# Performance work log

Measured on AMD Instinct MI355X. Metric: run time of the kernel, lower is better.

## Reference

```python
import jax, jax.numpy as jnp
import numpy as np


def setup_inputs() -> dict:
    key = jax.random.key(0)
    k1, k2, k3 = jax.random.split(key, 3)
    IN_C, OUT_C, K = 64, 64, 3
    x = jax.random.normal(k1, (16, IN_C, 256, 256), dtype=jnp.float32)
    # Conv2d weight (OIHW) and bias, Kaiming-ish scale
    fan_in = IN_C * K * K
    W = jax.random.normal(k2, (OUT_C, IN_C, K, K), dtype=jnp.float32) / np.sqrt(fan_in).astype(np.float32)
    b = jax.random.normal(k3, (OUT_C,), dtype=jnp.float32) * 0.01
    return {"x": x, "W": W, "b": b}


def reference(x, W, b):
    # The original module's quadruple Python loop multiplies each pixel by
    # mask(=1) * (1 - (h-1==h and w-1==w)) == 1, i.e. it is an identity.
    # The faithful math is therefore exactly Conv2d(k=3, padding=1) + bias.
    out = jax.lax.conv_general_dilated(
        x, W,
        window_strides=(1, 1),
        padding=((1, 1), (1, 1)),
        dimension_numbers=("NCHW", "OIHW", "NCHW"),
    )
    return out + b[None, :, None, None]
```

## Files before the change

kernel.cpp:

```cpp
#include <hip/hip_runtime.h>


#define N_   16
#define C_   64
#define HW_  256
#define TH   8
#define TW   32
#define NPIX ((TH + 2) * (TW + 2))
#define ICP  72

typedef __attribute__((ext_vector_type(8)))  short short8;
typedef __attribute__((ext_vector_type(16))) float f32x16;

static __device__ __forceinline__ unsigned short f2bf(float f) {
    unsigned u = __builtin_bit_cast(unsigned, f);
    return (unsigned short)((u + 0x7fffu + ((u >> 16) & 1u)) >> 16);
}

__global__ void repack_w_bf16(const float* __restrict__ W, unsigned short* __restrict__ Wt) {
    int i = blockIdx.x * 256 + threadIdx.x;
    if (i < C_ * 9 * C_) {
        int ic = i & 63, tap = (i >> 6) % 9, oc = (i >> 6) / 9;
        Wt[i] = f2bf(W[(oc * C_ + ic) * 9 + tap]);
    }
}

__global__ __launch_bounds__(256) void transpose_nhwc(const float* __restrict__ x,
                                                      unsigned short* __restrict__ xt) {
    __shared__ unsigned short st[64][ICP];
    const int tid = threadIdx.x;
    const int w0  = blockIdx.x * 64;
    const int h   = blockIdx.y;
    const int n   = blockIdx.z;

    #pragma unroll
    for (int k = 0; k < 4; ++k) {
        int i  = tid + k * 256;
        int ic = i >> 4, seg = i & 15;
        float4 v = *(const float4*)(x + (((size_t)(n * C_ + ic) * HW_ + h) * HW_ + w0 + seg * 4));
        st[seg * 4 + 0][ic] = f2bf(v.x);
        st[seg * 4 + 1][ic] = f2bf(v.y);
        st[seg * 4 + 2][ic] = f2bf(v.z);
        st[seg * 4 + 3][ic] = f2bf(v.w);
    }
    __syncthreads();
    #pragma unroll
    for (int j = 0; j < 2; ++j) {
        int w = (tid >> 3) + 32 * j, eg = tid & 7;
        uint4 v = *(const uint4*)&st[w][eg * 8];
        *(uint4*)(xt + (((size_t)n * HW_ + h) * HW_ + w0 + w) * C_ + eg * 8) = v;
    }
}

__global__ __launch_bounds__(256, 3) void conv_mfma_nhwc(const unsigned short* __restrict__ xt,
                                                         const unsigned short* __restrict__ Wt,
                                                         const float* __restrict__ bias,
                                                         float* __restrict__ out) {
    __shared__ unsigned short sx[NPIX][ICP];

    const int tid  = threadIdx.x;
    const int L    = tid & 63, wv = tid >> 6;
    const int half = L >> 5,  lm = L & 31;
    const int w0 = blockIdx.x * TW, h0 = blockIdx.y * TH, n = blockIdx.z;

    const unsigned short* xtn = xt + (size_t)n * HW_ * HW_ * C_;
    #pragma unroll
    for (int k = 0; k < 11; ++k) {
        int i = tid + k * 256;
        if (i < NPIX * 8) {
            int p = i >> 3, e = i & 7;
            int r = p / 34, col = p - r * 34;
            int gh = h0 + r - 1, gw = w0 + col - 1;
            uint4 v = make_uint4(0, 0, 0, 0);
            if ((unsigned)gh < HW_ && (unsigned)gw < HW_)
                v = *(const uint4*)(xtn + ((size_t)gh * HW_ + gw) * C_ + e * 8);
            *(uint4*)&sx[p][e * 8] = v;
        }
    }

    f32x16 acc00, acc01, acc10, acc11;
    #pragma unroll
    for (int r = 0; r < 16; ++r) {
        int ro = (r & 3) + 8 * (r >> 2) + 4 * half;
        float b0 = bias[ro], b1 = bias[32 + ro];
        acc00[r] = b0; acc01[r] = b0;
        acc10[r] = b1; acc11[r] = b1;
    }
    __syncthreads();

    const int r0 = 2 * wv;
    const unsigned short* wr0 = Wt + (0 * 32 + lm) * 576;
    const unsigned short* wr1 = Wt + (1 * 32 + lm) * 576;

    #pragma unroll
    for (int kh = 0; kh < 3; ++kh) {
        #pragma unroll
        for (int kw = 0; kw < 3; ++kw) {
            const int tap = kh * 3 + kw;
            const unsigned short* a0p = wr0 + tap * 64;
            const unsigned short* a1p = wr1 + tap * 64;
            const unsigned short* b0p = &sx[(r0 + kh) * 34 + lm + kw][0];
            const unsigned short* b1p = &sx[(r0 + 1 + kh) * 34 + lm + kw][0];
            #pragma unroll
            for (int s = 0; s < 4; ++s) {
                const int eo = s * 16 + half * 8;
                short8 a0 = __builtin_bit_cast(short8, *(const uint4*)(a0p + eo));
                short8 a1 = __builtin_bit_cast(short8, *(const uint4*)(a1p + eo));
                short8 b0 = __builtin_bit_cast(short8, *(const uint4*)(b0p + eo));
                short8 b1 = __builtin_bit_cast(short8, *(const uint4*)(b1p + eo));
                acc00 = __builtin_amdgcn_mfma_f32_32x32x16_bf16(a0, b0, acc00, 0, 0, 0);
                acc01 = __builtin_amdgcn_mfma_f32_32x32x16_bf16(a0, b1, acc01, 0, 0, 0);
                acc10 = __builtin_amdgcn_mfma_f32_32x32x16_bf16(a1, b0, acc10, 0, 0, 0);
                acc11 = __builtin_amdgcn_mfma_f32_32x32x16_bf16(a1, b1, acc11, 0, 0, 0);
            }
        }
    }

    float* outn = out + (size_t)n * C_ * HW_ * HW_;
    #pragma unroll
    for (int r = 0; r < 16; ++r) {
        int ro = (r & 3) + 8 * (r >> 2) + 4 * half;
        size_t base0 = ((size_t)ro        * HW_ + (h0 + r0)) * HW_ + w0 + lm;
        size_t base1 = ((size_t)(32 + ro) * HW_ + (h0 + r0)) * HW_ + w0 + lm;
        outn[base0]       = acc00[r];
        outn[base0 + HW_] = acc01[r];
        outn[base1]       = acc10[r];
        outn[base1 + HW_] = acc11[r];
    }
}

__global__ __launch_bounds__(256, 3) void conv_mfma_f32src(const float* __restrict__ x,
                                                           const unsigned short* __restrict__ Wt,
                                                           const float* __restrict__ bias,
                                                           float* __restrict__ out) {
    __shared__ unsigned short sx[NPIX][ICP];
    const int tid  = threadIdx.x;
    const int L    = tid & 63, wv = tid >> 6;
    const int half = L >> 5,  lm = L & 31;
    const int w0 = blockIdx.x * TW, h0 = blockIdx.y * TH, n = blockIdx.z;

    f32x16 acc00, acc01, acc10, acc11;
    #pragma unroll
    for (int r = 0; r < 16; ++r) {
        int ro = (r & 3) + 8 * (r >> 2) + 4 * half;
        float b0 = bias[ro], b1 = bias[32 + ro];
        acc00[r] = b0; acc01[r] = b0;
        acc10[r] = b1; acc11[r] = b1;
    }

    const float* xn = x + (size_t)n * C_ * HW_ * HW_;
    for (int c = tid; c < NPIX * 32; c += 256) {
        int icp = c / NPIX;
        int p   = c - icp * NPIX;
        int ph  = p / 34;
        int gh  = h0 + ph - 1, gw = w0 + (p - ph * 34) - 1;
        float v0 = 0.f, v1 = 0.f;
        if ((unsigned)gh < HW_ && (unsigned)gw < HW_) {
            const float* px = xn + ((size_t)(icp * 2) * HW_ + gh) * HW_ + gw;
            v0 = px[0];
            v1 = px[HW_ * HW_];
        }
        unsigned pk = (unsigned)f2bf(v0) | ((unsigned)f2bf(v1) << 16);
        *(unsigned*)&sx[p][icp * 2] = pk;
    }
    __syncthreads();

    const int r0 = 2 * wv;
    const unsigned short* wr0 = Wt + (0 * 32 + lm) * 576;
    const unsigned short* wr1 = Wt + (1 * 32 + lm) * 576;
    #pragma unroll
    for (int kh = 0; kh < 3; ++kh) {
        #pragma unroll
        for (int kw = 0; kw < 3; ++kw) {
            const int tap = kh * 3 + kw;
            const unsigned short* a0p = wr0 + tap * 64;
            const unsigned short* a1p = wr1 + tap * 64;
            const unsigned short* b0p = &sx[(r0 + kh) * 34 + lm + kw][0];
            const unsigned short* b1p = &sx[(r0 + 1 + kh) * 34 + lm + kw][0];
            #pragma unroll
            for (int s = 0; s < 4; ++s) {
                const int eo = s * 16 + half * 8;
                short8 a0 = __builtin_bit_cast(short8, *(const uint4*)(a0p + eo));
                short8 a1 = __builtin_bit_cast(short8, *(const uint4*)(a1p + eo));
                short8 b0 = __builtin_bit_cast(short8, *(const uint4*)(b0p + eo));
                short8 b1 = __builtin_bit_cast(short8, *(const uint4*)(b1p + eo));
                acc00 = __builtin_amdgcn_mfma_f32_32x32x16_bf16(a0, b0, acc00, 0, 0, 0);
                acc01 = __builtin_amdgcn_mfma_f32_32x32x16_bf16(a0, b1, acc01, 0, 0, 0);
                acc10 = __builtin_amdgcn_mfma_f32_32x32x16_bf16(a1, b0, acc10, 0, 0, 0);
                acc11 = __builtin_amdgcn_mfma_f32_32x32x16_bf16(a1, b1, acc11, 0, 0, 0);
            }
        }
    }

    float* outn = out + (size_t)n * C_ * HW_ * HW_;
    #pragma unroll
    for (int r = 0; r < 16; ++r) {
        int ro = (r & 3) + 8 * (r >> 2) + 4 * half;
        size_t base0 = ((size_t)ro        * HW_ + (h0 + r0)) * HW_ + w0 + lm;
        size_t base1 = ((size_t)(32 + ro) * HW_ + (h0 + r0)) * HW_ + w0 + lm;
        outn[base0]       = acc00[r];
        outn[base0 + HW_] = acc01[r];
        outn[base1]       = acc10[r];
        outn[base1 + HW_] = acc11[r];
    }
}

extern "C" void kernel_launch(void* const* d_in, const int* in_sizes, int n_in,
                              void* d_out, int out_size, void* d_ws, size_t ws_size,
                              hipStream_t stream) {
    const float* x = (const float*)d_in[0];
    const float* W = (const float*)d_in[1];
    const float* b = (const float*)d_in[2];
    float* out = (float*)d_out;

    dim3 grid(HW_ / TW, HW_ / TH, N_);
    dim3 block(256);

    const size_t xt_bytes = (size_t)N_ * HW_ * HW_ * C_ * sizeof(unsigned short);
    const size_t wt_bytes = (size_t)C_ * 9 * C_ * sizeof(unsigned short);

    if (ws_size >= xt_bytes + wt_bytes) {
        unsigned short* xt = (unsigned short*)d_ws;
        unsigned short* Wt = (unsigned short*)d_ws + xt_bytes / 2;
        repack_w_bf16<<<(C_ * 9 * C_ + 255) / 256, 256, 0, stream>>>(W, Wt);
        transpose_nhwc<<<dim3(4, HW_, N_), 256, 0, stream>>>(x, xt);
        conv_mfma_nhwc<<<grid, block, 0, stream>>>(xt, Wt, b, out);
    } else if (ws_size >= wt_bytes) {
        unsigned short* Wt = (unsigned short*)d_ws;
        repack_w_bf16<<<(C_ * 9 * C_ + 255) / 256, 256, 0, stream>>>(W, Wt);
        conv_mfma_f32src<<<grid, block, 0, stream>>>(x, Wt, b, out);
    }
}
```

Before: 644.3 us.

## Make conv persistent over row tiles with register-resident weights and prefetch

The conv kernel now runs 512-thread blocks that each loop over eight consecutive 8-row tiles. Each wave keeps its 32-output-channel weight slice in registers, and the next halo tile is prefetched into registers while the current one is computed, then written to shared memory between barriers. This cuts repeated weight loads from global memory and per-block launch and halo overhead. The transpose kernel also now packs channel pairs and uses an XOR-swizzled shared layout to reduce bank conflicts. In exchange the kernel carries a large register footprint (36 short8 weight fragments plus staging buffers), which may limit occupancy or cause spills.

Measured after the change: 588.8 us. 8.6% less time.

```diff
diff --git a/kernel.cpp b/kernel.cpp
--- a/kernel.cpp
+++ b/kernel.cpp
@@ -8,6 +8,7 @@
 #define TW   32
 #define NPIX ((TH + 2) * (TW + 2))
 #define ICP  72
+#define NT   8
 
 typedef __attribute__((ext_vector_type(8)))  short short8;
 typedef __attribute__((ext_vector_type(16))) float f32x16;
@@ -33,26 +34,35 @@
     const int h   = blockIdx.y;
     const int n   = blockIdx.z;
 
-    #pragma unroll
-    for (int k = 0; k < 4; ++k) {
-        int i  = tid + k * 256;
-        int ic = i >> 4, seg = i & 15;
-        float4 v = *(const float4*)(x + (((size_t)(n * C_ + ic) * HW_ + h) * HW_ + w0 + seg * 4));
-        st[seg * 4 + 0][ic] = f2bf(v.x);
-        st[seg * 4 + 1][ic] = f2bf(v.y);
-        st[seg * 4 + 2][ic] = f2bf(v.z);
-        st[seg * 4 + 3][ic] = f2bf(v.w);
+    const int seg = tid & 7;
+    const int icp = tid >> 3;
+    const int c   = icp >> 2, q = icp & 3;
+
+    #pragma unroll
+    for (int k = 0; k < 2; ++k) {
+        const float* p0 = x + (((size_t)(n * C_ + 2 * icp) * HW_ + h) * HW_ + w0 + k * 32 + seg * 4);
+        float4 a = *(const float4*)p0;
+        float4 b = *(const float4*)(p0 + (size_t)HW_ * HW_);
+        unsigned pk0 = (unsigned)f2bf(a.x) | ((unsigned)f2bf(b.x) << 16);
+        unsigned pk1 = (unsigned)f2bf(a.y) | ((unsigned)f2bf(b.y) << 16);
+        unsigned pk2 = (unsigned)f2bf(a.z) | ((unsigned)f2bf(b.z) << 16);
+        unsigned pk3 = (unsigned)f2bf(a.w) | ((unsigned)f2bf(b.w) << 16);
+        const int wb = k * 32 + seg * 4;
+        *(unsigned*)&st[wb + 0][(c ^ ((wb + 0) & 7)) * 8 + q * 2] = pk0;
+        *(unsigned*)&st[wb + 1][(c ^ ((wb + 1) & 7)) * 8 + q * 2] = pk1;
+        *(unsigned*)&st[wb + 2][(c ^ ((wb + 2) & 7)) * 8 + q * 2] = pk2;
+        *(unsigned*)&st[wb + 3][(c ^ ((wb + 3) & 7)) * 8 + q * 2] = pk3;
     }
     __syncthreads();
     #pragma unroll
     for (int j = 0; j < 2; ++j) {
         int w = (tid >> 3) + 32 * j, eg = tid & 7;
-        uint4 v = *(const uint4*)&st[w][eg * 8];
+        uint4 v = *(const uint4*)&st[w][(eg ^ (w & 7)) * 8];
         *(uint4*)(xt + (((size_t)n * HW_ + h) * HW_ + w0 + w) * C_ + eg * 8) = v;
     }
 }
 
-__global__ __launch_bounds__(256, 3) void conv_mfma_nhwc(const unsigned short* __restrict__ xt,
+__global__ __launch_bounds__(512, 2) void conv_mfma_wreg(const unsigned short* __restrict__ xt,
                                                          const unsigned short* __restrict__ Wt,
                                                          const float* __restrict__ bias,
                                                          float* __restrict__ out) {
@@ -61,71 +71,118 @@
     const int tid  = threadIdx.x;
     const int L    = tid & 63, wv = tid >> 6;
     const int half = L >> 5,  lm = L & 31;
-    const int w0 = blockIdx.x * TW, h0 = blockIdx.y * TH, n = blockIdx.z;
-
-    const unsigned short* xtn = xt + (size_t)n * HW_ * HW_ * C_;
-    #pragma unroll
-    for (int k = 0; k < 11; ++k) {
-        int i = tid + k * 256;
-        if (i < NPIX * 8) {
-            int p = i >> 3, e = i & 7;
-            int r = p / 34, col = p - r * 34;
-            int gh = h0 + r - 1, gw = w0 + col - 1;
-            uint4 v = make_uint4(0, 0, 0, 0);
-            if ((unsigned)gh < HW_ && (unsigned)gw < HW_)
-                v = *(const uint4*)(xtn + ((size_t)gh * HW_ + gw) * C_ + e * 8);
-            *(uint4*)&sx[p][e * 8] = v;
-        }
-    }
-
-    f32x16 acc00, acc01, acc10, acc11;
+    const int mg   = wv >> 2;
+    const int ng   = wv & 3;
+
+    const int bx = blockIdx.x;
+    const int wt = bx & 7, hg = (bx >> 3) & 3, n = bx >> 5;
+    const int w0 = wt * TW;
+
+    short8 wf[9][4];
+    {
+        const unsigned short* wbase = Wt + (size_t)(32 * mg + lm) * 576 + half * 8;
+        #pragma unroll
+        for (int tap = 0; tap < 9; ++tap)
+            #pragma unroll
+            for (int s = 0; s < 4; ++s)
+                wf[tap][s] = __builtin_bit_cast(short8, *(const uint4*)(wbase + tap * 64 + s * 16));
+    }
+    f32x16 bias_v;
     #pragma unroll
     for (int r = 0; r < 16; ++r) {
         int ro = (r & 3) + 8 * (r >> 2) + 4 * half;
-        float b0 = bias[ro], b1 = bias[32 + ro];
-        acc00[r] = b0; acc01[r] = b0;
-        acc10[r] = b1; acc11[r] = b1;
-    }
-    __syncthreads();
-
-    const int r0 = 2 * wv;
-    const unsigned short* wr0 = Wt + (0 * 32 + lm) * 576;
-    const unsigned short* wr1 = Wt + (1 * 32 + lm) * 576;
-
-    #pragma unroll
-    for (int kh = 0; kh < 3; ++kh) {
+        bias_v[r] = bias[32 * mg + ro];
+    }
+
+    const unsigned short* xtn = xt + (size_t)n * HW_ * HW_ * C_;
+    float* outn = out + (size_t)n * C_ * HW_ * HW_;
+    const unsigned short* pB = &sx[2 * ng * 34 + lm][half * 8];
+
+    {
+        const int h0 = hg * (NT * TH);
+        #pragma unroll
+        for (int k = 0; k < 6; ++k) {
+            int i = tid + k * 512;
+            if (i < NPIX * 8) {
+                int p = i >> 3, e = i & 7;
+                int r = p / 34, col = p - r * 34;
+                int gh = h0 + r - 1, gw = w0 + col - 1;
+                uint4 v = make_uint4(0, 0, 0, 0);
+                if ((unsigned)gh < HW_ && (unsigned)gw < HW_)
+                    v = *(const uint4*)(xtn + ((size_t)gh * HW_ + gw) * C_ + e * 8);
+                *(uint4*)&sx[p][e * 8] = v;
+            }
+        }
+    }
+    asm volatile("s_waitcnt lgkmcnt(0)" ::: "memory");
+    __builtin_amdgcn_sched_barrier(0);
+    __builtin_amdgcn_s_barrier();
+    __builtin_amdgcn_sched_barrier(0);
+
+    for (int t = 0; t < NT; ++t) {
+        const int h0 = hg * (NT * TH) + t * TH;
+
+        uint4 stg[6];
+        if (t < NT - 1) {
+            const int h1 = h0 + TH;
+            #pragma unroll
+            for (int k = 0; k < 6; ++k) {
+                int i = tid + k * 512;
+                stg[k] = make_uint4(0, 0, 0, 0);
+                if (i < NPIX * 8) {
+                    int p = i >> 3, e = i & 7;
+                    int r = p / 34, col = p - r * 34;
+                    int gh = h1 + r - 1, gw = w0 + col - 1;
+                    if ((unsigned)gh < HW_ && (unsigned)gw < HW_)
+                        stg[k] = *(const uint4*)(xtn + ((size_t)gh * HW_ + gw) * C_ + e * 8);
+                }
+            }
+        }
+
+        f32x16 acc0 = bias_v, acc1 = bias_v;
         #pragma unroll
         for (int kw = 0; kw < 3; ++kw) {
-            const int tap = kh * 3 + kw;
-            const unsigned short* a0p = wr0 + tap * 64;
-            const unsigned short* a1p = wr1 + tap * 64;
-            const unsigned short* b0p = &sx[(r0 + kh) * 34 + lm + kw][0];
-            const unsigned short* b1p = &sx[(r0 + 1 + kh) * 34 + lm + kw][0];
             #pragma unroll
             for (int s = 0; s < 4; ++s) {
-                const int eo = s * 16 + half * 8;
-                short8 a0 = __builtin_bit_cast(short8, *(const uint4*)(a0p + eo));
-                short8 a1 = __builtin_bit_cast(short8, *(const uint4*)(a1p + eo));
-                short8 b0 = __builtin_bit_cast(short8, *(const uint4*)(b0p + eo));
-                short8 b1 = __builtin_bit_cast(short8, *(const uint4*)(b1p + eo));
-                acc00 = __builtin_amdgcn_mfma_f32_32x32x16_bf16(a0, b0, acc00, 0, 0, 0);
-                acc01 = __builtin_amdgcn_mfma_f32_32x32x16_bf16(a0, b1, acc01, 0, 0, 0);
-                acc10 = __builtin_amdgcn_mfma_f32_32x32x16_bf16(a1, b0, acc10, 0, 0, 0);
-                acc11 = __builtin_amdgcn_mfma_f32_32x32x16_bf16(a1, b1, acc11, 0, 0, 0);
-            }
-        }
-    }
-
-    float* outn = out + (size_t)n * C_ * HW_ * HW_;
-    #pragma unroll
-    for (int r = 0; r < 16; ++r) {
-        int ro = (r & 3) + 8 * (r >> 2) + 4 * half;
-        size_t base0 = ((size_t)ro        * HW_ + (h0 + r0)) * HW_ + w0 + lm;
-        size_t base1 = ((size_t)(32 + ro) * HW_ + (h0 + r0)) * HW_ + w0 + lm;
-        outn[base0]       = acc00[r];
-        outn[base0 + HW_] = acc01[r];
-        outn[base1]       = acc10[r];
-        outn[base1 + HW_] = acc11[r];
+                short8 q0 = __builtin_bit_cast(short8, *(const uint4*)(pB + (0 * 34 + kw) * ICP + s * 16));
+                short8 q1 = __builtin_bit_cast(short8, *(const uint4*)(pB + (1 * 34 + kw) * ICP + s * 16));
+                short8 q2 = __builtin_bit_cast(short8, *(const uint4*)(pB + (2 * 34 + kw) * ICP + s * 16));
+                short8 q3 = __builtin_bit_cast(short8, *(const uint4*)(pB + (3 * 34 + kw) * ICP + s * 16));
+                acc0 = __builtin_amdgcn_mfma_f32_32x32x16_bf16(wf[0 * 3 + kw][s], q0, acc0, 0, 0, 0);
+                acc1 = __builtin_amdgcn_mfma_f32_32x32x16_bf16(wf[0 * 3 + kw][s], q1, acc1, 0, 0, 0);
+                acc0 = __builtin_amdgcn_mfma_f32_32x32x16_bf16(wf[1 * 3 + kw][s], q1, acc0, 0, 0, 0);
+                acc1 = __builtin_amdgcn_mfma_f32_32x32x16_bf16(wf[1 * 3 + kw][s], q2, acc1, 0, 0, 0);
+                acc0 = __builtin_amdgcn_mfma_f32_32x32x16_bf16(wf[2 * 3 + kw][s], q2, acc0, 0, 0, 0);
+                acc1 = __builtin_amdgcn_mfma_f32_32x32x16_bf16(wf[2 * 3 + kw][s], q3, acc1, 0, 0, 0);
+            }
+        }
+
+        const int row0 = h0 + 2 * ng;
+        #pragma unroll
+        for (int r = 0; r < 16; ++r) {
+            int ro = (r & 3) + 8 * (r >> 2) + 4 * half;
+            size_t base = ((size_t)(32 * mg + ro) * HW_ + row0) * HW_ + w0 + lm;
+            outn[base]       = acc0[r];
+            outn[base + HW_] = acc1[r];
+        }
+
+        if (t < NT - 1) {
+            __builtin_amdgcn_sched_barrier(0);
+            __builtin_amdgcn_s_barrier();
+            __builtin_amdgcn_sched_barrier(0);
+            #pragma unroll
+            for (int k = 0; k < 6; ++k) {
+                int i = tid + k * 512;
+                if (i < NPIX * 8) {
+                    int p = i >> 3, e = i & 7;
+                    *(uint4*)&sx[p][e * 8] = stg[k];
+                }
+            }
+            asm volatile("s_waitcnt lgkmcnt(0)" ::: "memory");
+            __builtin_amdgcn_sched_barrier(0);
+            __builtin_amdgcn_s_barrier();
+            __builtin_amdgcn_sched_barrier(0);
+        }
     }
 }
 
@@ -213,9 +270,6 @@
     const float* b = (const float*)d_in[2];
     float* out = (float*)d_out;
 
-    dim3 grid(HW_ / TW, HW_ / TH, N_);
-    dim3 block(256);
-
     const size_t xt_bytes = (size_t)N_ * HW_ * HW_ * C_ * sizeof(unsigned short);
     const size_t wt_bytes = (size_t)C_ * 9 * C_ * sizeof(unsigned short);
 
@@ -224,10 +278,10 @@
         unsigned short* Wt = (unsigned short*)d_ws + xt_bytes / 2;
         repack_w_bf16<<<(C_ * 9 * C_ + 255) / 256, 256, 0, stream>>>(W, Wt);
         transpose_nhwc<<<dim3(4, HW_, N_), 256, 0, stream>>>(x, xt);
-        conv_mfma_nhwc<<<grid, block, 0, stream>>>(xt, Wt, b, out);
+        conv_mfma_wreg<<<dim3(512), dim3(512), 0, stream>>>(xt, Wt, b, out);
     } else if (ws_size >= wt_bytes) {
         unsigned short* Wt = (unsigned short*)d_ws;
         repack_w_bf16<<<(C_ * 9 * C_ + 255) / 256, 256, 0, stream>>>(W, Wt);
-        conv_mfma_f32src<<<grid, block, 0, stream>>>(x, Wt, b, out);
-    }
-}
+        conv_mfma_f32src<<<dim3(HW_ / TW, HW_ / TH, N_), 256, 0, stream>>>(x, Wt, b, out);
+    }
+}
```
